# Kernel optimization log

Measured on AMD Instinct MI355X. Metric: run time of the kernel, lower is better.

The kernel has to match this reference:

```python
import jax, jax.numpy as jnp
import numpy as np

N = 100000
E = 600000
IN_DIM, HID_DIM, OUT_DIM = 128, 64, 3


def setup_inputs() -> dict:
    key = jax.random.key(0)
    ks = jax.random.split(key, 8)
    x = jax.random.normal(ks[0], (N, IN_DIM), dtype=jnp.float32)
    edge_index = jax.random.randint(ks[1], (2, E), 0, N, dtype=jnp.int64)
    # SAGEConv layer 1: lin_l (neighbors, with bias), lin_r (root, no bias)
    s1 = 1.0 / np.sqrt(IN_DIM)
    Wl1 = jax.random.uniform(ks[2], (IN_DIM, HID_DIM), jnp.float32, -s1, s1)
    Wr1 = jax.random.uniform(ks[3], (IN_DIM, HID_DIM), jnp.float32, -s1, s1)
    b1 = jnp.zeros((HID_DIM,), jnp.float32)
    # SAGEConv layer 2
    s2 = 1.0 / np.sqrt(HID_DIM)
    Wl2 = jax.random.uniform(ks[4], (HID_DIM, OUT_DIM), jnp.float32, -s2, s2)
    Wr2 = jax.random.uniform(ks[5], (HID_DIM, OUT_DIM), jnp.float32, -s2, s2)
    b2 = jnp.zeros((OUT_DIM,), jnp.float32)
    return {"x": x, "edge_index": edge_index,
            "Wl1": Wl1, "Wr1": Wr1, "b1": b1,
            "Wl2": Wl2, "Wr2": Wr2, "b2": b2}


def _mean_aggregate(h, src, dst, num_nodes):
    # mean of source-node features over incoming edges per destination node
    summed = jax.ops.segment_sum(h[src], dst, num_segments=num_nodes)  # [N, F]
    cnt = jax.ops.segment_sum(jnp.ones((src.shape[0],), h.dtype), dst,
                              num_segments=num_nodes)
    return summed / jnp.maximum(cnt, 1.0)[:, None]


def _sage_conv(h, src, dst, Wl, Wr, b, num_nodes):
    # PyG SAGEConv (aggr='mean'): lin_l(mean_j x_j) + lin_r(x_i)
    agg = _mean_aggregate(h, src, dst, num_nodes)
    return agg @ Wl + h @ Wr + b


def reference(x, edge_index, Wl1, Wr1, b1, Wl2, Wr2, b2):
    src, dst = edge_index[0], edge_index[1]  # flow: source_to_target
    n = x.shape[0]
    h = jax.nn.relu(_sage_conv(x, src, dst, Wl1, Wr1, b1, n))
    out = _sage_conv(h, src, dst, Wl2, Wr2, b2, n)
    return jax.nn.log_softmax(out, axis=1)
```

## Files before the change

kernel.cpp:

```cpp
#include <hip/hip_runtime.h>
#include <hip/hip_bf16.h>

#define IN_DIM 128
#define HID 64
#define SCAN_B 1024
#define WSTR 136
#define CB 512

using half8 = __attribute__((ext_vector_type(8))) _Float16;
using half2v = __attribute__((ext_vector_type(2))) _Float16;
using f32x4 = __attribute__((ext_vector_type(4))) float;

__global__ __launch_bounds__(256) void init_kernel(
    const float* __restrict__ Wl, const float* __restrict__ Wr,
    _Float16* __restrict__ wcatT, int4* __restrict__ deg4, int n4,
    int* __restrict__ gcur) {
  const int i = blockIdx.x * 256 + threadIdx.x;
  if (i == 0) *gcur = 0;
  if (i < 16384) {
    const int col = i >> 7;
    const int k = i & 127;
    const float v = (col < 64) ? Wl[k * HID + col] : Wr[k * HID + col - 64];
    wcatT[col * 128 + k] = (_Float16)v;
  }
  if (i < n4) deg4[i] = (int4){0, 0, 0, 0};
}

__global__ __launch_bounds__(256) void proj1_count_kernel(
    const float* __restrict__ x, const _Float16* __restrict__ wcatT,
    _Float16* __restrict__ xW, _Float16* __restrict__ xWr, int N, int ntiles,
    const int* __restrict__ ei, int* __restrict__ deg_i,
    int* __restrict__ eoff, int E) {
  const int tx = threadIdx.x;
  if (blockIdx.x >= ntiles) {
    const int nb = gridDim.x - ntiles;
    for (int e = (blockIdx.x - ntiles) * 256 + tx; e < E; e += nb * 256)
      eoff[e] = atomicAdd(&deg_i[ei[E + e]], 1);
    return;
  }
  __shared__ _Float16 wsT[128][WSTR];

#pragma unroll
  for (int it = 0; it < 8; ++it) {
    const int e8 = it * 256 + tx;
    const int col = e8 >> 4;
    const int k8 = (e8 & 15) * 8;
    *(half8*)&wsT[col][k8] = *(const half8*)&wcatT[col * 128 + k8];
  }

  const int lane = tx & 63;
  const int wv = tx >> 6;
  const int lrow = lane & 15;
  const int g = lane >> 4;
  const float4* x4 = (const float4*)x;

  const int n0 = blockIdx.x * 64;
  const int row = n0 + wv * 16 + lrow;

  __syncthreads();

  f32x4 acc[8];
#pragma unroll
  for (int ct = 0; ct < 8; ++ct) acc[ct] = (f32x4){0.f, 0.f, 0.f, 0.f};

#pragma unroll
  for (int kt = 0; kt < 4; ++kt) {
    half8 a;
    if (row < N) {
      const float4 u = x4[(size_t)row * 32 + kt * 8 + g * 2];
      const float4 v = x4[(size_t)row * 32 + kt * 8 + g * 2 + 1];
      a[0] = (_Float16)u.x; a[1] = (_Float16)u.y;
      a[2] = (_Float16)u.z; a[3] = (_Float16)u.w;
      a[4] = (_Float16)v.x; a[5] = (_Float16)v.y;
      a[6] = (_Float16)v.z; a[7] = (_Float16)v.w;
    } else {
      a = (half8){0, 0, 0, 0, 0, 0, 0, 0};
    }
#pragma unroll
    for (int ct = 0; ct < 8; ++ct) {
      const half8 b = *(const half8*)&wsT[ct * 16 + lrow][kt * 32 + g * 8];
      acc[ct] = __builtin_amdgcn_mfma_f32_16x16x32_f16(a, b, acc[ct], 0, 0, 0);
    }
  }

#pragma unroll
  for (int ct = 0; ct < 8; ++ct) {
    const int col = ct * 16 + lrow;
#pragma unroll
    for (int reg = 0; reg < 4; ++reg) {
      const int nn = n0 + wv * 16 + g * 4 + reg;
      if (nn < N) {
        if (col < 64)
          xW[(size_t)nn * HID + col] = (_Float16)acc[ct][reg];
        else
          xWr[(size_t)nn * HID + col - 64] = (_Float16)acc[ct][reg];
      }
    }
  }
}

__global__ __launch_bounds__(SCAN_B) void scan_kernel(
    const int* __restrict__ deg_i, int* __restrict__ row_off,
    int* __restrict__ gcur, int n) {
  __shared__ int s[SCAN_B];
  __shared__ int base;
  const int t = threadIdx.x;
  const int i = blockIdx.x * SCAN_B + t;
  const int v = (i < n) ? deg_i[i] : 0;
  s[t] = v;
  for (int off = 1; off < SCAN_B; off <<= 1) {
    __syncthreads();
    const int a = (t >= off) ? s[t - off] : 0;
    __syncthreads();
    s[t] += a;
  }
  if (t == SCAN_B - 1) base = atomicAdd(gcur, s[SCAN_B - 1]);
  __syncthreads();
  if (i < n) row_off[i] = base + s[t] - v;
}

__global__ __launch_bounds__(256) void fill_kernel(
    const int* __restrict__ ei, const int* __restrict__ row_off,
    const int* __restrict__ eoff, int* __restrict__ csr_src, int E) {
  const int e = blockIdx.x * blockDim.x + threadIdx.x;
  if (e < E) {
    const int s = ei[e];
    const int d = ei[E + e];
    atomicExch(&csr_src[row_off[d] + eoff[e]], s);
  }
}

__global__ __launch_bounds__(256) void layer1_kernel(
    const int* __restrict__ row_off, const int* __restrict__ deg_i,
    const int* __restrict__ csr_src, const _Float16* __restrict__ xW,
    const _Float16* __restrict__ xWr, const float* __restrict__ b1,
    const float* __restrict__ Wl2, const float* __restrict__ Wr2,
    float* __restrict__ pl, float* __restrict__ pr, int N, int ntiles) {
  __shared__ _Float16 wlds[16][72];
  __shared__ _Float16 hlds[64][72];
  const int tx = threadIdx.x;
  for (int i = tx; i < 1024; i += 256) {
    const int c = i >> 6;
    const int k = i & 63;
    float v = 0.f;
    if (c < 3) v = Wl2[k * 3 + c];
    else if (c < 6) v = Wr2[k * 3 + (c - 3)];
    wlds[c][k] = (_Float16)v;
  }
  const int lane = tx & 63;
  const int wv = tx >> 6;
  const int lrow = lane & 15;
  const int g = lane >> 4;
  const int half = lane >> 5;
  const int c2 = lane & 31;
  const float2 bb2 = *(const float2*)&b1[2 * c2];
  const half2v* xW2 = (const half2v*)xW;
  const half2v* xWr2 = (const half2v*)xWr;
  __syncthreads();

#pragma unroll 1
  for (int tile = blockIdx.x; tile < ntiles; tile += gridDim.x) {
    const int base = tile * 64;
#pragma unroll 1
    for (int p = 0; p < 8; ++p) {
      const int nl = 2 * p + half;
      const int myN = base + wv * 16 + nl;
      float a0x = 0.f, a0y = 0.f, a1x = 0.f, a1y = 0.f;
      float a2x = 0.f, a2y = 0.f, a3x = 0.f, a3y = 0.f;
      int start = 0, dg = 0;
      if (myN < N) {
        start = row_off[myN];
        dg = deg_i[myN];
      }
      int r = 0;
      for (; r + 3 < dg; r += 4) {
        const int s0 = csr_src[start + r];
        const int s1 = csr_src[start + r + 1];
        const int s2 = csr_src[start + r + 2];
        const int s3 = csr_src[start + r + 3];
        const half2v v0 = xW2[(size_t)s0 * 32 + c2];
        const half2v v1 = xW2[(size_t)s1 * 32 + c2];
        const half2v v2 = xW2[(size_t)s2 * 32 + c2];
        const half2v v3 = xW2[(size_t)s3 * 32 + c2];
        a0x += (float)v0.x; a0y += (float)v0.y;
        a1x += (float)v1.x; a1y += (float)v1.y;
        a2x += (float)v2.x; a2y += (float)v2.y;
        a3x += (float)v3.x; a3y += (float)v3.y;
      }
      for (; r < dg; ++r) {
        const half2v v0 = xW2[(size_t)csr_src[start + r] * 32 + c2];
        a0x += (float)v0.x; a0y += (float)v0.y;
      }
      const float dinv = 1.0f / fmaxf((float)dg, 1.0f);
      half2v wr = {0, 0};
      if (myN < N) wr = xWr2[(size_t)myN * 32 + c2];
      const float hx =
          fmaxf(((a0x + a1x) + (a2x + a3x)) * dinv + (float)wr.x + bb2.x, 0.f);
      const float hy =
          fmaxf(((a0y + a1y) + (a2y + a3y)) * dinv + (float)wr.y + bb2.y, 0.f);
      half2v hv;
      hv.x = (_Float16)hx;
      hv.y = (_Float16)hy;
      *(half2v*)&hlds[wv * 16 + nl][2 * c2] = hv;
    }
    __syncthreads();
    f32x4 acc = (f32x4){0.f, 0.f, 0.f, 0.f};
#pragma unroll
    for (int kt = 0; kt < 2; ++kt) {
      const half8 a = *(const half8*)&hlds[wv * 16 + lrow][kt * 32 + g * 8];
      const half8 b = *(const half8*)&wlds[lrow][kt * 32 + g * 8];
      acc = __builtin_amdgcn_mfma_f32_16x16x32_f16(a, b, acc, 0, 0, 0);
    }
    if (lrow < 6) {
#pragma unroll
      for (int reg = 0; reg < 4; ++reg) {
        const int n = base + wv * 16 + g * 4 + reg;
        if (n < N) {
          if (lrow < 3)
            pl[(size_t)n * 3 + lrow] = acc[reg];
          else
            pr[(size_t)n * 3 + lrow - 3] = acc[reg];
        }
      }
    }
    __syncthreads();
  }
}

__global__ __launch_bounds__(256) void final_kernel(
    const int* __restrict__ row_off, const int* __restrict__ deg_i,
    const int* __restrict__ csr_src, const float* __restrict__ pl,
    const float* __restrict__ pr, const float* __restrict__ b2,
    float* __restrict__ out, int N) {
  const int stride = gridDim.x * blockDim.x;
  const float b20 = b2[0], b21 = b2[1], b22 = b2[2];
  for (int n = blockIdx.x * blockDim.x + threadIdx.x; n < N; n += stride) {
    const int start = row_off[n];
    const int dg = deg_i[n];
    float s0 = 0.f, s1 = 0.f, s2 = 0.f;
    float t0 = 0.f, t1 = 0.f, t2 = 0.f;
    int r = 0;
    for (; r + 1 < dg; r += 2) {
      const int sa = csr_src[start + r];
      const int sb = csr_src[start + r + 1];
      s0 += pl[(size_t)sa * 3 + 0];
      s1 += pl[(size_t)sa * 3 + 1];
      s2 += pl[(size_t)sa * 3 + 2];
      t0 += pl[(size_t)sb * 3 + 0];
      t1 += pl[(size_t)sb * 3 + 1];
      t2 += pl[(size_t)sb * 3 + 2];
    }
    if (r < dg) {
      const int sa = csr_src[start + r];
      s0 += pl[(size_t)sa * 3 + 0];
      s1 += pl[(size_t)sa * 3 + 1];
      s2 += pl[(size_t)sa * 3 + 2];
    }
    const float dinv = 1.0f / fmaxf((float)dg, 1.0f);
    const float v0 = (s0 + t0) * dinv + pr[(size_t)n * 3 + 0] + b20;
    const float v1 = (s1 + t1) * dinv + pr[(size_t)n * 3 + 1] + b21;
    const float v2 = (s2 + t2) * dinv + pr[(size_t)n * 3 + 2] + b22;
    const float m = fmaxf(fmaxf(v0, v1), v2);
    const float e0 = __expf(v0 - m), e1 = __expf(v1 - m), e2 = __expf(v2 - m);
    const float lse = __logf(e0 + e1 + e2);
    out[(size_t)n * 3 + 0] = v0 - m - lse;
    out[(size_t)n * 3 + 1] = v1 - m - lse;
    out[(size_t)n * 3 + 2] = v2 - m - lse;
  }
}

extern "C" void kernel_launch(void* const* d_in, const int* in_sizes, int n_in,
                              void* d_out, int out_size, void* d_ws,
                              size_t ws_size, hipStream_t stream) {
  const float* x = (const float*)d_in[0];
  const int* ei = (const int*)d_in[1];
  const float* Wl1 = (const float*)d_in[2];
  const float* Wr1 = (const float*)d_in[3];
  const float* b1 = (const float*)d_in[4];
  const float* Wl2 = (const float*)d_in[5];
  const float* Wr2 = (const float*)d_in[6];
  const float* b2 = (const float*)d_in[7];
  float* out = (float*)d_out;

  const int N = in_sizes[0] / IN_DIM;
  const int E = in_sizes[1] / 2;
  const int nb1 = (N + SCAN_B - 1) / SCAN_B;
  const int ntiles = (N + 63) / 64;

  int* wsI = (int*)d_ws;
  int* deg_i = wsI;
  int* row_off = deg_i + N;
  int* gcur = row_off + N;
  int* eoff = gcur + 4;
  int* csr_src = eoff + E;
  _Float16* wcatT = (_Float16*)(csr_src + E);
  _Float16* xW = wcatT + 128 * 128;
  _Float16* xWr = xW + (size_t)N * HID;
  float* pl = (float*)(xWr + (size_t)N * HID);
  float* pr = pl + (size_t)N * 3;

  const int n4 = (N + 3) / 4;
  const int initg = (max(n4, 16384) + 255) / 256;
  init_kernel<<<initg, 256, 0, stream>>>(Wl1, Wr1, wcatT, (int4*)deg_i, n4,
                                         gcur);
  proj1_count_kernel<<<ntiles + CB, 256, 0, stream>>>(
      x, wcatT, xW, xWr, N, ntiles, ei, deg_i, eoff, E);
  scan_kernel<<<nb1, SCAN_B, 0, stream>>>(deg_i, row_off, gcur, N);
  fill_kernel<<<(E + 255) / 256, 256, 0, stream>>>(ei, row_off, eoff, csr_src,
                                                   E);
  layer1_kernel<<<ntiles, 256, 0, stream>>>(row_off, deg_i, csr_src, xW, xWr,
                                            b1, Wl2, Wr2, pl, pr, N, ntiles);
  final_kernel<<<(N + 255) / 256, 256, 0, stream>>>(row_off, deg_i, csr_src,
                                                    pl, pr, b2, out, N);
}
```

Baseline: 118.3 us.

## Fuse projection with CSR fill and pack layer-2 neighbor projections as half4

The layer-1 projection GEMM moves out of the degree-count kernel and into the CSR fill kernel. Extra blocks in that kernel do the scatter, so the fill overlaps with the GEMM instead of the count, and counting becomes a plain standalone kernel. The layer-2 neighbor projections are stored as padded fp16 half4 rows, so each gather in the final kernel is one 8-byte load instead of three scattered 4-byte loads. This trades some precision in the aggregated logits for less gather traffic.

```diff
diff --git a/kernel.cpp b/kernel.cpp
--- a/kernel.cpp
+++ b/kernel.cpp
@@ -5,9 +5,10 @@
 #define HID 64
 #define SCAN_B 1024
 #define WSTR 136
-#define CB 512
+#define FB 512
 
 using half8 = __attribute__((ext_vector_type(8))) _Float16;
+using half4 = __attribute__((ext_vector_type(4))) _Float16;
 using half2v = __attribute__((ext_vector_type(2))) _Float16;
 using f32x4 = __attribute__((ext_vector_type(4))) float;
 
@@ -26,77 +27,12 @@
   if (i < n4) deg4[i] = (int4){0, 0, 0, 0};
 }
 
-__global__ __launch_bounds__(256) void proj1_count_kernel(
-    const float* __restrict__ x, const _Float16* __restrict__ wcatT,
-    _Float16* __restrict__ xW, _Float16* __restrict__ xWr, int N, int ntiles,
-    const int* __restrict__ ei, int* __restrict__ deg_i,
-    int* __restrict__ eoff, int E) {
-  const int tx = threadIdx.x;
-  if (blockIdx.x >= ntiles) {
-    const int nb = gridDim.x - ntiles;
-    for (int e = (blockIdx.x - ntiles) * 256 + tx; e < E; e += nb * 256)
-      eoff[e] = atomicAdd(&deg_i[ei[E + e]], 1);
-    return;
-  }
-  __shared__ _Float16 wsT[128][WSTR];
-
-#pragma unroll
-  for (int it = 0; it < 8; ++it) {
-    const int e8 = it * 256 + tx;
-    const int col = e8 >> 4;
-    const int k8 = (e8 & 15) * 8;
-    *(half8*)&wsT[col][k8] = *(const half8*)&wcatT[col * 128 + k8];
-  }
-
-  const int lane = tx & 63;
-  const int wv = tx >> 6;
-  const int lrow = lane & 15;
-  const int g = lane >> 4;
-  const float4* x4 = (const float4*)x;
-
-  const int n0 = blockIdx.x * 64;
-  const int row = n0 + wv * 16 + lrow;
-
-  __syncthreads();
-
-  f32x4 acc[8];
-#pragma unroll
-  for (int ct = 0; ct < 8; ++ct) acc[ct] = (f32x4){0.f, 0.f, 0.f, 0.f};
-
-#pragma unroll
-  for (int kt = 0; kt < 4; ++kt) {
-    half8 a;
-    if (row < N) {
-      const float4 u = x4[(size_t)row * 32 + kt * 8 + g * 2];
-      const float4 v = x4[(size_t)row * 32 + kt * 8 + g * 2 + 1];
-      a[0] = (_Float16)u.x; a[1] = (_Float16)u.y;
-      a[2] = (_Float16)u.z; a[3] = (_Float16)u.w;
-      a[4] = (_Float16)v.x; a[5] = (_Float16)v.y;
-      a[6] = (_Float16)v.z; a[7] = (_Float16)v.w;
-    } else {
-      a = (half8){0, 0, 0, 0, 0, 0, 0, 0};
-    }
-#pragma unroll
-    for (int ct = 0; ct < 8; ++ct) {
-      const half8 b = *(const half8*)&wsT[ct * 16 + lrow][kt * 32 + g * 8];
-      acc[ct] = __builtin_amdgcn_mfma_f32_16x16x32_f16(a, b, acc[ct], 0, 0, 0);
-    }
-  }
-
-#pragma unroll
-  for (int ct = 0; ct < 8; ++ct) {
-    const int col = ct * 16 + lrow;
-#pragma unroll
-    for (int reg = 0; reg < 4; ++reg) {
-      const int nn = n0 + wv * 16 + g * 4 + reg;
-      if (nn < N) {
-        if (col < 64)
-          xW[(size_t)nn * HID + col] = (_Float16)acc[ct][reg];
-        else
-          xWr[(size_t)nn * HID + col - 64] = (_Float16)acc[ct][reg];
-      }
-    }
-  }
+__global__ __launch_bounds__(256) void count_kernel(const int* __restrict__ ei,
+                                                    int* __restrict__ deg_i,
+                                                    int* __restrict__ eoff,
+                                                    int E) {
+  const int e = blockIdx.x * blockDim.x + threadIdx.x;
+  if (e < E) eoff[e] = atomicAdd(&deg_i[ei[E + e]], 1);
 }
 
 __global__ __launch_bounds__(SCAN_B) void scan_kernel(
@@ -119,14 +55,79 @@
   if (i < n) row_off[i] = base + s[t] - v;
 }
 
-__global__ __launch_bounds__(256) void fill_kernel(
+__global__ __launch_bounds__(256) void proj1_fill_kernel(
+    const float* __restrict__ x, const _Float16* __restrict__ wcatT,
+    _Float16* __restrict__ xW, _Float16* __restrict__ xWr, int N, int ntiles,
     const int* __restrict__ ei, const int* __restrict__ row_off,
     const int* __restrict__ eoff, int* __restrict__ csr_src, int E) {
-  const int e = blockIdx.x * blockDim.x + threadIdx.x;
-  if (e < E) {
-    const int s = ei[e];
-    const int d = ei[E + e];
-    atomicExch(&csr_src[row_off[d] + eoff[e]], s);
+  const int tx = threadIdx.x;
+  if (blockIdx.x >= ntiles) {
+    const int nb = gridDim.x - ntiles;
+    for (int e = (blockIdx.x - ntiles) * 256 + tx; e < E; e += nb * 256) {
+      const int s = ei[e];
+      const int d = ei[E + e];
+      atomicExch(&csr_src[row_off[d] + eoff[e]], s);
+    }
+    return;
+  }
+  __shared__ _Float16 wsT[128][WSTR];
+
+#pragma unroll
+  for (int it = 0; it < 8; ++it) {
+    const int e8 = it * 256 + tx;
+    const int col = e8 >> 4;
+    const int k8 = (e8 & 15) * 8;
+    *(half8*)&wsT[col][k8] = *(const half8*)&wcatT[col * 128 + k8];
+  }
+
+  const int lane = tx & 63;
+  const int wv = tx >> 6;
+  const int lrow = lane & 15;
+  const int g = lane >> 4;
+  const float4* x4 = (const float4*)x;
+
+  const int n0 = blockIdx.x * 64;
+  const int row = n0 + wv * 16 + lrow;
+
+  __syncthreads();
+
+  f32x4 acc[8];
+#pragma unroll
+  for (int ct = 0; ct < 8; ++ct) acc[ct] = (f32x4){0.f, 0.f, 0.f, 0.f};
+
+#pragma unroll
+  for (int kt = 0; kt < 4; ++kt) {
+    half8 a;
+    if (row < N) {
+      const float4 u = x4[(size_t)row * 32 + kt * 8 + g * 2];
+      const float4 v = x4[(size_t)row * 32 + kt * 8 + g * 2 + 1];
+      a[0] = (_Float16)u.x; a[1] = (_Float16)u.y;
+      a[2] = (_Float16)u.z; a[3] = (_Float16)u.w;
+      a[4] = (_Float16)v.x; a[5] = (_Float16)v.y;
+      a[6] = (_Float16)v.z; a[7] = (_Float16)v.w;
+    } else {
+      a = (half8){0, 0, 0, 0, 0, 0, 0, 0};
+    }
+#pragma unroll
+    for (int ct = 0; ct < 8; ++ct) {
+      const half8 b = *(const half8*)&wsT[ct * 16 + lrow][kt * 32 + g * 8];
+      acc[ct] = __builtin_amdgcn_mfma_f32_16x16x32_f16(a, b, acc[ct], 0, 0, 0);
+    }
+  }
+
+#pragma unroll
+  for (int ct = 0; ct < 8; ++ct) {
+    const int col = ct * 16 + lrow;
+#pragma unroll
+    for (int reg = 0; reg < 4; ++reg) {
+      const int nn = n0 + wv * 16 + g * 4 + reg;
+      if (nn < N) {
+        if (col < 64)
+          xW[(size_t)nn * HID + col] = (_Float16)acc[ct][reg];
+        else
+          xWr[(size_t)nn * HID + col - 64] = (_Float16)acc[ct][reg];
+      }
+    }
   }
 }
 
@@ -135,7 +136,7 @@
     const int* __restrict__ csr_src, const _Float16* __restrict__ xW,
     const _Float16* __restrict__ xWr, const float* __restrict__ b1,
     const float* __restrict__ Wl2, const float* __restrict__ Wr2,
-    float* __restrict__ pl, float* __restrict__ pr, int N, int ntiles) {
+    _Float16* __restrict__ pl4, float* __restrict__ pr, int N, int ntiles) {
   __shared__ _Float16 wlds[16][72];
   __shared__ _Float16 hlds[64][72];
   const int tx = threadIdx.x;
@@ -217,7 +218,7 @@
         const int n = base + wv * 16 + g * 4 + reg;
         if (n < N) {
           if (lrow < 3)
-            pl[(size_t)n * 3 + lrow] = acc[reg];
+            pl4[(size_t)n * 4 + lrow] = (_Float16)acc[reg];
           else
             pr[(size_t)n * 3 + lrow - 3] = acc[reg];
         }
@@ -229,11 +230,12 @@
 
 __global__ __launch_bounds__(256) void final_kernel(
     const int* __restrict__ row_off, const int* __restrict__ deg_i,
-    const int* __restrict__ csr_src, const float* __restrict__ pl,
+    const int* __restrict__ csr_src, const _Float16* __restrict__ pl4,
     const float* __restrict__ pr, const float* __restrict__ b2,
     float* __restrict__ out, int N) {
   const int stride = gridDim.x * blockDim.x;
   const float b20 = b2[0], b21 = b2[1], b22 = b2[2];
+  const half4* p4 = (const half4*)pl4;
   for (int n = blockIdx.x * blockDim.x + threadIdx.x; n < N; n += stride) {
     const int start = row_off[n];
     const int dg = deg_i[n];
@@ -241,20 +243,14 @@
     float t0 = 0.f, t1 = 0.f, t2 = 0.f;
     int r = 0;
     for (; r + 1 < dg; r += 2) {
-      const int sa = csr_src[start + r];
-      const int sb = csr_src[start + r + 1];
-      s0 += pl[(size_t)sa * 3 + 0];
-      s1 += pl[(size_t)sa * 3 + 1];
-      s2 += pl[(size_t)sa * 3 + 2];
-      t0 += pl[(size_t)sb * 3 + 0];
-      t1 += pl[(size_t)sb * 3 + 1];
-      t2 += pl[(size_t)sb * 3 + 2];
+      const half4 va = p4[csr_src[start + r]];
+      const half4 vb = p4[csr_src[start + r + 1]];
+      s0 += (float)va[0]; s1 += (float)va[1]; s2 += (float)va[2];
+      t0 += (float)vb[0]; t1 += (float)vb[1]; t2 += (float)vb[2];
     }
     if (r < dg) {
-      const int sa = csr_src[start + r];
-      s0 += pl[(size_t)sa * 3 + 0];
-      s1 += pl[(size_t)sa * 3 + 1];
-      s2 += pl[(size_t)sa * 3 + 2];
+      const half4 va = p4[csr_src[start + r]];
+      s0 += (float)va[0]; s1 += (float)va[1]; s2 += (float)va[2];
     }
     const float dinv = 1.0f / fmaxf((float)dg, 1.0f);
     const float v0 = (s0 + t0) * dinv + pr[(size_t)n * 3 + 0] + b20;
@@ -296,20 +292,19 @@
   _Float16* wcatT = (_Float16*)(csr_src + E);
   _Float16* xW = wcatT + 128 * 128;
   _Float16* xWr = xW + (size_t)N * HID;
-  float* pl = (float*)(xWr + (size_t)N * HID);
-  float* pr = pl + (size_t)N * 3;
+  _Float16* pl4 = xWr + (size_t)N * HID;
+  float* pr = (float*)(pl4 + (size_t)N * 4);
 
   const int n4 = (N + 3) / 4;
   const int initg = (max(n4, 16384) + 255) / 256;
   init_kernel<<<initg, 256, 0, stream>>>(Wl1, Wr1, wcatT, (int4*)deg_i, n4,
                                          gcur);
-  proj1_count_kernel<<<ntiles + CB, 256, 0, stream>>>(
-      x, wcatT, xW, xWr, N, ntiles, ei, deg_i, eoff, E);
+  count_kernel<<<(E + 255) / 256, 256, 0, stream>>>(ei, deg_i, eoff, E);
   scan_kernel<<<nb1, SCAN_B, 0, stream>>>(deg_i, row_off, gcur, N);
-  fill_kernel<<<(E + 255) / 256, 256, 0, stream>>>(ei, row_off, eoff, csr_src,
-                                                   E);
+  proj1_fill_kernel<<<ntiles + FB, 256, 0, stream>>>(
+      x, wcatT, xW, xWr, N, ntiles, ei, row_off, eoff, csr_src, E);
   layer1_kernel<<<ntiles, 256, 0, stream>>>(row_off, deg_i, csr_src, xW, xWr,
-                                            b1, Wl2, Wr2, pl, pr, N, ntiles);
+                                            b1, Wl2, Wr2, pl4, pr, N, ntiles);
   final_kernel<<<(N + 255) / 256, 256, 0, stream>>>(row_off, deg_i, csr_src,
-                                                    pl, pr, b2, out, N);
-}
+                                                    pl4, pr, b2, out, N);
+}
```

Measured after the change: 117.6 us. Within noise of the previous version (-0.6%).
